# Kernel tuning notes

Measured on AMD Instinct MI355X. Metric: run time of the kernel, lower is better.

The kernel has to match this reference:

```python
import jax, jax.numpy as jnp
import numpy as np

BITS = 4
GROUP = 128
IN_F = 4096
OUT_F = 4096
N_TOK = 8192
N_STAGES = 4
QMAX = 2 ** BITS - 1  # affine (sym=False)


def _round_ste(x):
    return x + jax.lax.stop_gradient(jnp.round(x) - x)


def _clamp_ste(x, lo, hi):
    return x + jax.lax.stop_gradient(jnp.clip(x, lo, hi) - x)


def apply_rotation(x, pairs, theta, group_size):
    # x: [N, H]; pairs: [R, H] int (per-group index pairs in [0, group_size));
    # theta: [R, H//2]
    n, h = x.shape
    g = h // group_size
    half = group_size // 2
    offsets = (jnp.arange(g, dtype=jnp.int32) * group_size)[:, None]  # [G,1]
    pair_view = pairs.reshape(pairs.shape[0], g, half, 2)
    theta_view = theta.reshape(theta.shape[0], g, half)
    out = x
    for r in range(pairs.shape[0]):  # small fixed number of rotation stages
        idx_i = (pair_view[r, :, :, 0] + offsets).reshape(-1)  # [H//2]
        idx_j = (pair_view[r, :, :, 1] + offsets).reshape(-1)
        xi = out[:, idx_i]  # [N, H//2]
        xj = out[:, idx_j]
        c = jnp.cos(theta_view[r]).reshape(-1)[None, :]
        s = jnp.sin(theta_view[r]).reshape(-1)[None, :]
        out = out.at[:, idx_i].set(xi * c + xj * s).at[:, idx_j].set(-xi * s + xj * c)
    return out


def quant_dequant_affine_ste(w, scale, zero_point_float, group_size):
    # pseudo_quantize_dequant with sym=False, use_ste=True
    view = w.reshape(-1, group_size)
    s = _clamp_ste(scale, 1e-5, 1e5)
    rzp = _clamp_ste(-_round_ste(zero_point_float), 0.0, float(QMAX))
    q = _round_ste(view / s) + rzp
    q = _clamp_ste(q, 0.0, float(QMAX))
    return ((q - rzp) * s).reshape(w.shape)


def setup_inputs() -> dict:
    key = jax.random.key(0)
    k1, k2, k3, k4 = jax.random.split(key, 4)
    x = jax.random.normal(k1, (N_TOK, IN_F), dtype=jnp.float32)
    weight = jax.random.normal(k2, (OUT_F, IN_F), dtype=jnp.float32) * 0.02
    bias = jax.random.normal(k3, (OUT_F,), dtype=jnp.float32) * 0.01
    channel_scales = jnp.ones((IN_F,), dtype=jnp.float32)
    theta = jax.random.normal(k4, (N_STAGES, IN_F // 2), dtype=jnp.float32) * 0.05
    # per-group pair permutations: each stage/group is a permutation of [0, GROUP)
    rng = np.random.default_rng(0)
    g = IN_F // GROUP
    pairs_np = np.stack([
        np.concatenate([rng.permutation(GROUP) for _ in range(g)])
        for _ in range(N_STAGES)
    ]).astype(np.int32)  # [R, IN_F]
    pairs = jnp.asarray(pairs_np)
    # affine qparams from initial (theta=0, scales=1) transformed weight == weight
    view = weight.reshape(-1, GROUP)
    min_val = view.min(axis=1, keepdims=True)
    max_val = view.max(axis=1, keepdims=True)
    q_scale = jnp.clip(max_val - min_val, 1e-5, None) / QMAX
    q_zero_point = min_val / q_scale
    theta_mask = jnp.ones((N_STAGES, IN_F // 2), dtype=bool)
    return {"x": x, "weight": weight, "bias": bias,
            "channel_scales": channel_scales, "theta": theta,
            "q_scale": q_scale, "q_zero_point": q_zero_point,
            "pairs": pairs, "theta_mask": theta_mask}


def reference(x, weight, bias, channel_scales, theta, q_scale, q_zero_point, pairs, theta_mask):
    # transformed_weight(): scale input channels then group-wise Givens rotate
    w_scaled = weight * channel_scales[None, :]
    w_t = apply_rotation(w_scaled, pairs, theta, GROUP)
    # STE pseudo quantize-dequantize in the transformed domain
    w_q = quant_dequant_affine_ste(w_t, q_scale, q_zero_point, GROUP)
    # inverse rotation back to the original input domain, undo channel scales
    w_back = apply_rotation(w_q, pairs[::-1], -theta[::-1], GROUP) / channel_scales[None, :]
    return x @ w_back.T + bias[None, :]
```

## Files before the change

kernel.cpp:

```cpp
#include <hip/hip_runtime.h>
#include <hip/hip_bf16.h>
#include <math.h>

#define IN_F    4096
#define OUT_F   4096
#define N_TOK   8192
#define GROUP   128
#define NSTAGE  4
#define NPAIRS  2048
#define QMAXF   15.0

typedef unsigned short u16;
typedef __bf16 bf16x8 __attribute__((ext_vector_type(8)));
typedef float  f32x4  __attribute__((ext_vector_type(4)));

struct alignas(8) U16x4 { u16 x, y, z, w; };

__device__ __forceinline__ u16 f2bf(float f) {
    unsigned u = __float_as_uint(f);
    unsigned r = (u + 0x7fffu + ((u >> 16) & 1u)) >> 16;
    return (u16)r;
}

__device__ __forceinline__ void gl_lds16(const void* g, void* l) {
    __builtin_amdgcn_global_load_lds(
        (const __attribute__((address_space(1))) void*)g,
        (__attribute__((address_space(3))) void*)l,
        16, 0, 0);
}

__device__ __forceinline__ void bar() {
    asm volatile("" ::: "memory");
    __builtin_amdgcn_s_barrier();
    asm volatile("" ::: "memory");
}

__global__ void make_tabs(const float* __restrict__ theta,
                          double* __restrict__ ctab, double* __restrict__ stab) {
    int i = blockIdx.x * 256 + threadIdx.x;
    if (i < NSTAGE * NPAIRS) {
        double t = (double)theta[i];
        ctab[i] = cos(t);
        stab[i] = sin(t);
    }
}

__global__ __launch_bounds__(256) void build_w(
    const float* __restrict__ weight, const float* __restrict__ cs,
    const float* __restrict__ qs, const float* __restrict__ qzp,
    const int* __restrict__ pairs,
    const double* __restrict__ ctab, const double* __restrict__ stab,
    u16* __restrict__ wb) {
    __shared__ double gbuf[4][GROUP];
    const int wave = threadIdx.x >> 6, l = threadIdx.x & 63;
    const int task = blockIdx.x * 4 + wave;
    const int o = task >> 5, g = task & 31;
    double* gb = gbuf[wave];
    const int e0 = g * GROUP;

    float2 wv = *(const float2*)(weight + (size_t)o * IN_F + e0 + 2 * l);
    float2 cv = *(const float2*)(cs + e0 + 2 * l);
    gb[2 * l]     = (double)wv.x * (double)cv.x;
    gb[2 * l + 1] = (double)wv.y * (double)cv.y;
    __builtin_amdgcn_wave_barrier();

    const int2* prs = (const int2*)pairs;

    for (int r = 0; r < NSTAGE; ++r) {
        int2 p = prs[r * (IN_F / 2) + g * 64 + l];
        double c = ctab[r * NPAIRS + g * 64 + l];
        double s = stab[r * NPAIRS + g * 64 + l];
        double xi = gb[p.x], xj = gb[p.y];
        __builtin_amdgcn_wave_barrier();
        gb[p.x] =  xi * c + xj * s;
        gb[p.y] = -xi * s + xj * c;
        __builtin_amdgcn_wave_barrier();
    }

    {
        double s   = fmin(fmax((double)qs[o * 32 + g], 1e-5), 1e5);
        double rzp = fmin(fmax(-rint((double)qzp[o * 32 + g]), 0.0), QMAXF);
#pragma unroll
        for (int e = 2 * l; e <= 2 * l + 1; ++e) {
            double q = rint(gb[e] / s) + rzp;
            q = fmin(fmax(q, 0.0), QMAXF);
            gb[e] = (q - rzp) * s;
        }
        __builtin_amdgcn_wave_barrier();
    }

    for (int r = NSTAGE - 1; r >= 0; --r) {
        int2 p = prs[r * (IN_F / 2) + g * 64 + l];
        double c = ctab[r * NPAIRS + g * 64 + l];
        double s = stab[r * NPAIRS + g * 64 + l];
        double xi = gb[p.x], xj = gb[p.y];
        __builtin_amdgcn_wave_barrier();
        gb[p.x] = xi * c - xj * s;
        gb[p.y] = xi * s + xj * c;
        __builtin_amdgcn_wave_barrier();
    }

    unsigned lo = f2bf((float)(gb[2 * l]     / (double)cv.x));
    unsigned hi = f2bf((float)(gb[2 * l + 1] / (double)cv.y));
    *(unsigned*)(wb + (size_t)o * IN_F + e0 + 2 * l) = lo | (hi << 16);
}

__global__ void cast_x(const float* __restrict__ x, u16* __restrict__ xb) {
    size_t i = ((size_t)blockIdx.x * 256 + threadIdx.x) * 4;
    float4 v = *(const float4*)(x + i);
    U16x4 o;
    o.x = f2bf(v.x); o.y = f2bf(v.y); o.z = f2bf(v.z); o.w = f2bf(v.w);
    *(U16x4*)(xb + i) = o;
}

__global__ __launch_bounds__(512, 2) void gemm_bt(
    const u16* __restrict__ A, const u16* __restrict__ B,
    const float* __restrict__ bias, float* __restrict__ C) {
    constexpr int K = IN_F;
    constexpr int N = OUT_F;
    constexpr int NGRP = K / 64;
    constexpr int TIL = 256 * 64;
    __shared__ __align__(16) u16 As[2][TIL];
    __shared__ __align__(16) u16 Bs[2][TIL];

    const int tid  = threadIdx.x;
    const int wave = tid >> 6, lane = tid & 63;
    const int lrow = lane & 15, lq = lane >> 4;
    const int wm = wave >> 2, wn = wave & 3;

    const int wg = (blockIdx.x & 7) * 64 + (blockIdx.x >> 3);
    const int mt = wg & 31, nt = wg >> 5;
    const int m0 = mt * 256, n0 = nt * 256;

    const int prow = tid >> 3;
    const int pch  = (tid & 7) ^ ((tid >> 3) & 7);
    const u16* pA = A + (size_t)(m0 + prow) * K + pch * 8;
    const u16* pB = B + (size_t)(n0 + prow) * K + pch * 8;

#define STAGE_A(slot, t) do {                                                  \
        _Pragma("unroll")                                                      \
        for (int hr_ = 0; hr_ < 4; ++hr_) {                                    \
            const int h_ = hr_ >> 1, r_ = hr_ & 1;                             \
            gl_lds16(pA + (size_t)(h_ * 128 + r_ * 64) * K + (t) * 64,         \
                     &As[slot][h_ * 8192 + r_ * 4096 + (wave << 9)]);          \
        }                                                                      \
    } while (0)
#define STAGE_B(slot, t) do {                                                  \
        _Pragma("unroll")                                                      \
        for (int hr_ = 0; hr_ < 4; ++hr_) {                                    \
            const int h_ = hr_ >> 1, r_ = hr_ & 1;                             \
            gl_lds16(pB + (size_t)(h_ * 128 + r_ * 64) * K + (t) * 64,         \
                     &Bs[slot][h_ * 8192 + r_ * 4096 + (wave << 9)]);          \
        }                                                                      \
    } while (0)

#define RD_A(ks) do {                                                          \
        _Pragma("unroll")                                                      \
        for (int mi_ = 0; mi_ < 8; ++mi_) {                                    \
            const int ar_ = (wm << 7) + (mi_ << 4) + lrow;                     \
            af[mi_] = *(const bf16x8*)&as_[(ar_ << 6) +                        \
                (((((ks) << 2) | lq) ^ (ar_ & 7)) << 3)];                      \
        }                                                                      \
    } while (0)
#define RD_B(ks, nj0) do {                                                     \
        const int br0_ = (wn << 6) + ((nj0) << 4) + lrow;                      \
        b0 = *(const bf16x8*)&bs_[(br0_ << 6) +                                \
                (((((ks) << 2) | lq) ^ (br0_ & 7)) << 3)];                     \
        b1 = *(const bf16x8*)&bs_[((br0_ + 16) << 6) +                         \
                (((((ks) << 2) | lq) ^ (br0_ & 7)) << 3)];                     \
    } while (0)

#define MF2(nj0) do {                                                          \
        __builtin_amdgcn_s_setprio(1);                                         \
        _Pragma("unroll")                                                      \
        for (int mi_ = 0; mi_ < 8; ++mi_) {                                    \
            acc[mi_][nj0] = __builtin_amdgcn_mfma_f32_16x16x32_bf16(           \
                af[mi_], b0, acc[mi_][nj0], 0, 0, 0);                          \
            acc[mi_][(nj0) + 1] = __builtin_amdgcn_mfma_f32_16x16x32_bf16(     \
                af[mi_], b1, acc[mi_][(nj0) + 1], 0, 0, 0);                    \
        }                                                                      \
        __builtin_amdgcn_s_setprio(0);                                         \
    } while (0)

    f32x4 acc[8][4];
#pragma unroll
    for (int i = 0; i < 8; ++i)
#pragma unroll
        for (int j = 0; j < 4; ++j) acc[i][j] = (f32x4){0.f, 0.f, 0.f, 0.f};

    STAGE_A(0, 0); STAGE_B(0, 0); STAGE_A(1, 1); STAGE_B(1, 1);
    asm volatile("s_waitcnt vmcnt(8)" ::: "memory");
    __builtin_amdgcn_s_barrier();
    asm volatile("" ::: "memory");

#pragma unroll 2
    for (int g = 0; g < NGRP; ++g) {
        u16* as_ = As[g & 1];
        u16* bs_ = Bs[g & 1];
        bf16x8 af[8], b0, b1;

        RD_A(0);
        RD_B(0, 0);
        if (g >= 1 && g + 1 < NGRP) STAGE_B((g + 1) & 1, g + 1);
        bar();
        MF2(0);
        bar();

        RD_B(0, 2);
        bar();
        MF2(2);
        bar();

        RD_A(1);
        RD_B(1, 0);
        bar();
        MF2(0);
        bar();

        RD_B(1, 2);
        if (g + 2 < NGRP) {
            STAGE_A(g & 1, g + 2);
            asm volatile("s_waitcnt vmcnt(4)" ::: "memory");
        } else if (g + 1 < NGRP) {
            asm volatile("s_waitcnt vmcnt(0)" ::: "memory");
        }
        bar();
        MF2(2);
        bar();
    }

#undef STAGE_A
#undef STAGE_B
#undef RD_A
#undef RD_B
#undef MF2

#pragma unroll
    for (int mi = 0; mi < 8; ++mi) {
        int rb = m0 + wm * 128 + mi * 16 + lq * 4;
#pragma unroll
        for (int nj = 0; nj < 4; ++nj) {
            int col = n0 + wn * 64 + nj * 16 + lrow;
            float bv = bias[col];
#pragma unroll
            for (int r = 0; r < 4; ++r)
                C[(size_t)(rb + r) * N + col] = acc[mi][nj][r] + bv;
        }
    }
}

extern "C" void kernel_launch(void* const* d_in, const int* in_sizes, int n_in,
                              void* d_out, int out_size, void* d_ws, size_t ws_size,
                              hipStream_t stream) {
    const float* x    = (const float*)d_in[0];
    const float* w    = (const float*)d_in[1];
    const float* bias = (const float*)d_in[2];
    const float* cs   = (const float*)d_in[3];
    const float* th   = (const float*)d_in[4];
    const float* qs   = (const float*)d_in[5];
    const float* qzp  = (const float*)d_in[6];
    const int*   pr   = (const int*)d_in[7];
    float* out = (float*)d_out;

    char* ws = (char*)d_ws;
    double* ctab = (double*)ws;
    double* stab = (double*)(ws + 65536);
    u16*    xb   = (u16*)(ws + 131072);
    u16*    wb   = (u16*)(ws + 131072 + (size_t)N_TOK * IN_F * 2);

    hipLaunchKernelGGL(make_tabs, dim3((NSTAGE * NPAIRS + 255) / 256), dim3(256),
                       0, stream, th, ctab, stab);
    hipLaunchKernelGGL(build_w, dim3(OUT_F * 32 / 4), dim3(256), 0, stream,
                       w, cs, qs, qzp, pr, ctab, stab, wb);
    hipLaunchKernelGGL(cast_x, dim3(N_TOK * IN_F / 4 / 256), dim3(256), 0, stream,
                       x, xb);
    hipLaunchKernelGGL(gemm_bt, dim3((N_TOK / 256) * (OUT_F / 256)), dim3(512),
                       0, stream, xb, wb, bias, out);
}
```

Measured before the change: 672.6 us.

## Restructure GEMM main loop into quadrant MFMA phases with split staging

Reorganizes the bf16 GEMM inner loop so each K-tile is processed as four quadrant MFMA blocks (M-half by N-half, both k-steps), with A and B fragments for both k-substeps loaded up front. The global-to-LDS staging is split into half-tile chunks interleaved across the four phases, so loads are spread more evenly against compute. This aims to improve fragment reuse and overlap of loads with MFMA, at the cost of more live registers (a0/a1/b0/b1 arrays) and a changed vmcnt accounting that must stay correct.

```diff
diff --git a/kernel.cpp b/kernel.cpp
--- a/kernel.cpp
+++ b/kernel.cpp
@@ -118,10 +118,9 @@
     const float* __restrict__ bias, float* __restrict__ C) {
     constexpr int K = IN_F;
     constexpr int N = OUT_F;
-    constexpr int NGRP = K / 64;
-    constexpr int TIL = 256 * 64;
-    __shared__ __align__(16) u16 As[2][TIL];
-    __shared__ __align__(16) u16 Bs[2][TIL];
+    constexpr int NT = K / 64;
+    __shared__ __align__(16) u16 As[2][256 * 64];
+    __shared__ __align__(16) u16 Bs[2][256 * 64];
 
     const int tid  = threadIdx.x;
     const int wave = tid >> 6, lane = tid & 63;
@@ -137,48 +136,52 @@
     const u16* pA = A + (size_t)(m0 + prow) * K + pch * 8;
     const u16* pB = B + (size_t)(n0 + prow) * K + pch * 8;
 
-#define STAGE_A(slot, t) do {                                                  \
-        _Pragma("unroll")                                                      \
-        for (int hr_ = 0; hr_ < 4; ++hr_) {                                    \
-            const int h_ = hr_ >> 1, r_ = hr_ & 1;                             \
-            gl_lds16(pA + (size_t)(h_ * 128 + r_ * 64) * K + (t) * 64,         \
-                     &As[slot][h_ * 8192 + r_ * 4096 + (wave << 9)]);          \
+#define STG_A(s, t, h) do {                                                    \
+        gl_lds16(pA + (size_t)((h) * 128) * K + (t) * 64,                      \
+                 &As[s][(h) * 8192 + (wave << 9)]);                            \
+        gl_lds16(pA + (size_t)((h) * 128 + 64) * K + (t) * 64,                 \
+                 &As[s][(h) * 8192 + 4096 + (wave << 9)]);                     \
+    } while (0)
+#define STG_B(s, t, h) do {                                                    \
+        gl_lds16(pB + (size_t)((h) * 128) * K + (t) * 64,                      \
+                 &Bs[s][(h) * 8192 + (wave << 9)]);                            \
+        gl_lds16(pB + (size_t)((h) * 128 + 64) * K + (t) * 64,                 \
+                 &Bs[s][(h) * 8192 + 4096 + (wave << 9)]);                     \
+    } while (0)
+
+#define RD_A(dst, mih) do {                                                    \
+        _Pragma("unroll")                                                      \
+        for (int ks_ = 0; ks_ < 2; ++ks_)                                      \
+        _Pragma("unroll")                                                      \
+        for (int j_ = 0; j_ < 4; ++j_) {                                       \
+            const int ar_ = (wm << 7) + ((mih) << 6) + (j_ << 4) + lrow;       \
+            dst[ks_ * 4 + j_] = *(const bf16x8*)&as_[(ar_ << 6) +              \
+                ((((ks_ << 2) | lq) ^ (ar_ & 7)) << 3)];                       \
         }                                                                      \
     } while (0)
-#define STAGE_B(slot, t) do {                                                  \
-        _Pragma("unroll")                                                      \
-        for (int hr_ = 0; hr_ < 4; ++hr_) {                                    \
-            const int h_ = hr_ >> 1, r_ = hr_ & 1;                             \
-            gl_lds16(pB + (size_t)(h_ * 128 + r_ * 64) * K + (t) * 64,         \
-                     &Bs[slot][h_ * 8192 + r_ * 4096 + (wave << 9)]);          \
+#define RD_B(dst, njh) do {                                                    \
+        _Pragma("unroll")                                                      \
+        for (int ks_ = 0; ks_ < 2; ++ks_)                                      \
+        _Pragma("unroll")                                                      \
+        for (int j_ = 0; j_ < 2; ++j_) {                                       \
+            const int br_ = (wn << 6) + ((njh) << 5) + (j_ << 4) + lrow;       \
+            dst[ks_ * 2 + j_] = *(const bf16x8*)&bs_[(br_ << 6) +              \
+                ((((ks_ << 2) | lq) ^ (br_ & 7)) << 3)];                       \
         }                                                                      \
     } while (0)
 
-#define RD_A(ks) do {                                                          \
-        _Pragma("unroll")                                                      \
-        for (int mi_ = 0; mi_ < 8; ++mi_) {                                    \
-            const int ar_ = (wm << 7) + (mi_ << 4) + lrow;                     \
-            af[mi_] = *(const bf16x8*)&as_[(ar_ << 6) +                        \
-                (((((ks) << 2) | lq) ^ (ar_ & 7)) << 3)];                      \
-        }                                                                      \
-    } while (0)
-#define RD_B(ks, nj0) do {                                                     \
-        const int br0_ = (wn << 6) + ((nj0) << 4) + lrow;                      \
-        b0 = *(const bf16x8*)&bs_[(br0_ << 6) +                                \
-                (((((ks) << 2) | lq) ^ (br0_ & 7)) << 3)];                     \
-        b1 = *(const bf16x8*)&bs_[((br0_ + 16) << 6) +                         \
-                (((((ks) << 2) | lq) ^ (br0_ & 7)) << 3)];                     \
-    } while (0)
-
-#define MF2(nj0) do {                                                          \
+#define MFQ(am, bn, mih, njh) do {                                             \
         __builtin_amdgcn_s_setprio(1);                                         \
         _Pragma("unroll")                                                      \
-        for (int mi_ = 0; mi_ < 8; ++mi_) {                                    \
-            acc[mi_][nj0] = __builtin_amdgcn_mfma_f32_16x16x32_bf16(           \
-                af[mi_], b0, acc[mi_][nj0], 0, 0, 0);                          \
-            acc[mi_][(nj0) + 1] = __builtin_amdgcn_mfma_f32_16x16x32_bf16(     \
-                af[mi_], b1, acc[mi_][(nj0) + 1], 0, 0, 0);                    \
-        }                                                                      \
+        for (int ks_ = 0; ks_ < 2; ++ks_)                                      \
+        _Pragma("unroll")                                                      \
+        for (int j_ = 0; j_ < 4; ++j_)                                         \
+        _Pragma("unroll")                                                      \
+        for (int n_ = 0; n_ < 2; ++n_)                                         \
+            acc[((mih) << 2) + j_][((njh) << 1) + n_] =                        \
+                __builtin_amdgcn_mfma_f32_16x16x32_bf16(                       \
+                    am[ks_ * 4 + j_], bn[ks_ * 2 + n_],                        \
+                    acc[((mih) << 2) + j_][((njh) << 1) + n_], 0, 0, 0);       \
         __builtin_amdgcn_s_setprio(0);                                         \
     } while (0)
 
@@ -188,52 +191,52 @@
 #pragma unroll
         for (int j = 0; j < 4; ++j) acc[i][j] = (f32x4){0.f, 0.f, 0.f, 0.f};
 
-    STAGE_A(0, 0); STAGE_B(0, 0); STAGE_A(1, 1); STAGE_B(1, 1);
-    asm volatile("s_waitcnt vmcnt(8)" ::: "memory");
+    STG_A(0, 0, 0); STG_A(0, 0, 1); STG_B(0, 0, 0); STG_B(0, 0, 1);
+    STG_A(1, 1, 0); STG_A(1, 1, 1);
+    asm volatile("s_waitcnt vmcnt(4)" ::: "memory");
     __builtin_amdgcn_s_barrier();
     asm volatile("" ::: "memory");
 
-#pragma unroll 2
-    for (int g = 0; g < NGRP; ++g) {
-        u16* as_ = As[g & 1];
-        u16* bs_ = Bs[g & 1];
-        bf16x8 af[8], b0, b1;
-
-        RD_A(0);
-        RD_B(0, 0);
-        if (g >= 1 && g + 1 < NGRP) STAGE_B((g + 1) & 1, g + 1);
-        bar();
-        MF2(0);
-        bar();
-
-        RD_B(0, 2);
-        bar();
-        MF2(2);
-        bar();
-
-        RD_A(1);
-        RD_B(1, 0);
-        bar();
-        MF2(0);
-        bar();
-
-        RD_B(1, 2);
-        if (g + 2 < NGRP) {
-            STAGE_A(g & 1, g + 2);
+    for (int u = 0; u < NT; ++u) {
+        const u16* as_ = As[u & 1];
+        const u16* bs_ = Bs[u & 1];
+        bf16x8 a0[8], a1[8], b0[4], b1[4];
+
+        RD_A(a0, 0);
+        RD_B(b0, 0);
+        if (u < NT - 1) STG_B((u + 1) & 1, u + 1, 0);
+        bar();
+        MFQ(a0, b0, 0, 0);
+        bar();
+
+        RD_A(a1, 1);
+        if (u < NT - 1) STG_B((u + 1) & 1, u + 1, 1);
+        bar();
+        MFQ(a1, b0, 1, 0);
+        bar();
+
+        RD_B(b1, 1);
+        if (u < NT - 2) STG_A(u & 1, u + 2, 0);
+        bar();
+        MFQ(a0, b1, 0, 1);
+        bar();
+
+        if (u < NT - 2) {
+            STG_A(u & 1, u + 2, 1);
             asm volatile("s_waitcnt vmcnt(4)" ::: "memory");
-        } else if (g + 1 < NGRP) {
+        } else if (u == NT - 2) {
             asm volatile("s_waitcnt vmcnt(0)" ::: "memory");
         }
         bar();
-        MF2(2);
-        bar();
-    }
-
-#undef STAGE_A
-#undef STAGE_B
+        MFQ(a1, b1, 1, 1);
+        bar();
+    }
+
+#undef STG_A
+#undef STG_B
 #undef RD_A
 #undef RD_B
-#undef MF2
+#undef MFQ
 
 #pragma unroll
     for (int mi = 0; mi < 8; ++mi) {
```

New measurement: 687.8 us. 2.3% more time.
